# Performance work log

Hardware: AMD Instinct MI355X
Metric: run time of the kernel (lower is better)

## Reference

```python
import jax, jax.numpy as jnp
import numpy as np

B, N, E, S, ANN_D, N_STEPS = 16384, 70, 3, 10, 1, 5


def setup_inputs() -> dict:
    key = jax.random.key(0)
    ks = jax.random.split(key, 10)
    std = 0.02
    annotation = jax.random.normal(ks[0], (B, N), jnp.float32)
    A_raw = jax.random.uniform(ks[1], (N, N * E), jnp.float32) + 1e-3
    A = A_raw / A_raw.sum(axis=1, keepdims=True)  # row-normalized like torch.div(A, sum(A,1))
    W_in = jax.random.normal(ks[2], (E, S, S), jnp.float32) * std
    b_in = jnp.zeros((E, S), jnp.float32)
    Wr = jax.random.normal(ks[3], (S, 2 * S), jnp.float32) * std
    br = jnp.zeros((S,), jnp.float32)
    Wz = jax.random.normal(ks[4], (S, 2 * S), jnp.float32) * std
    bz = jnp.zeros((S,), jnp.float32)
    Wh = jax.random.normal(ks[5], (S, 2 * S), jnp.float32) * std
    bh = jnp.zeros((S,), jnp.float32)
    Wo1 = jax.random.normal(ks[6], (S, S + ANN_D), jnp.float32) * std
    bo1 = jnp.zeros((S,), jnp.float32)
    Wo2 = jax.random.normal(ks[7], (1, S), jnp.float32) * std
    bo2 = jnp.zeros((1,), jnp.float32)
    return {"annotation": annotation, "A": A, "W_in": W_in, "b_in": b_in,
            "Wr": Wr, "br": br, "Wz": Wz, "bz": bz, "Wh": Wh, "bh": bh,
            "Wo1": Wo1, "bo1": bo1, "Wo2": Wo2, "bo2": bo2}


def reference(annotation, A, W_in, b_in, Wr, br, Wz, bz, Wh, bh, Wo1, bo1, Wo2, bo2):
    b, n = annotation.shape
    ann = annotation[..., None]  # [B, N, 1]
    # initial state: annotation padded with zeros to state_dim
    prop = jnp.concatenate([ann, jnp.zeros((b, n, S - ANN_D), annotation.dtype)], axis=2)  # [B,N,S]
    for _ in range(N_STEPS):
        # per-edge-type linear: [B,E,N,S]; view order is edge-type-major (matches torch stack/transpose/view)
        ins = jnp.einsum('bnd,efd->benf', prop, W_in) + b_in[None, :, None, :]
        ins = ins.reshape(b, E * n, S)  # [B, E*N, S]
        a_in = jnp.einsum('nm,bms->bns', A, ins)  # bmm aggregation, [B,N,S]
        a = jnp.concatenate([a_in, prop], axis=2)  # [B,N,2S]
        r = jax.nn.sigmoid(a @ Wr.T + br)
        z = jax.nn.sigmoid(a @ Wz.T + bz)
        joined = jnp.concatenate([a_in, r * prop], axis=2)
        h_hat = jnp.tanh(joined @ Wh.T + bh)
        prop = (1.0 - z) * prop + z * h_hat
    join_state = jnp.concatenate([prop, ann], axis=2)  # [B,N,S+1]
    out = jnp.tanh(join_state @ Wo1.T + bo1) @ Wo2.T + bo2  # [B,N,1]
    return out.sum(axis=2)  # [B,N]
```

## Files before the change

### kernel.cpp

```cpp
#include <hip/hip_runtime.h>
#include <hip/hip_bf16.h>

typedef _Float16 v8h __attribute__((ext_vector_type(8)));
typedef _Float16 v4h __attribute__((ext_vector_type(4)));
typedef _Float16 v2h __attribute__((ext_vector_type(2)));
typedef float    v4f __attribute__((ext_vector_type(4)));

#define NTOT  16384
#define NN    70
#define STEPS 5
#define TPB   64
#define NBLK  NTOT
#define CATN  40
#define CATH  3208
#define USTR  232
#define UH    (10*USTR)

#define PWO1 0
#define PWO2 120
#define PBO2 130
#define NWP  132

#define OFR  1024
#define OFZ  1536
#define OFH  2048
#define OFA  2560
#define NWF  20480
#define PREPB 40

__device__ __align__(16) float    g_w[NWP];
__device__ __align__(16) _Float16 g_wf[NWF];
__device__ int g_flag;

__device__ __forceinline__ float fast_sigmoid(float x) {
    return __builtin_amdgcn_rcpf(1.0f + __expf(-x));
}
__device__ __forceinline__ float fast_tanh(float x) {
    float ax = fabsf(x);
    float e  = __expf(-2.0f * ax);
    float t  = (1.0f - e) * __builtin_amdgcn_rcpf(1.0f + e);
    return copysignf(t, x);
}

struct __align__(16) Smem {
    _Float16 U[UH];
    _Float16 cat[CATH];
};

__global__ void prep_kernel(const void* annv, const void* Av,
    const void* winv, const void* binv, const void* wrv, const void* brv,
    const void* wzv, const void* bzv, const void* whv, const void* bhv,
    const void* wo1v, const void* bo1v, const void* wo2v, const void* bo2v)
{
    __shared__ int sflag;
    if (threadIdx.x == 0) {
        const unsigned short* u = (const unsigned short*)annv;
        int good = 0;
        for (int k = 0; k < 128; ++k) {
            unsigned short bb = u[k];
            int ex = (bb >> 7) & 0xFF;
            if (bb == 0 || (ex >= 101 && ex <= 131)) ++good;
        }
        sflag = (good >= 112) ? 1 : 0;
        if (blockIdx.x == 0) g_flag = sflag;
    }
    __syncthreads();
    const int f = sflag;
    #define RD(p, i) (f ? (float)((const __hip_bfloat16*)(p))[i] : ((const float*)(p))[i])
    const int tid = threadIdx.x;
    if (blockIdx.x == 0) {
        for (int idx = tid; idx < 120; idx += blockDim.x) {
            const int s = idx / 12, cc = idx - s*12;
            g_w[PWO1 + idx] = (cc < 11) ? RD(wo1v, s*11 + cc) : RD(bo1v, s);
        }
        for (int idx = tid; idx < 10; idx += blockDim.x) g_w[PWO2 + idx] = RD(wo2v, idx);
        if (tid == 0) { g_w[PBO2] = RD(bo2v, 0); g_w[PBO2+1] = 0.f; }
    }
    for (int idx = blockIdx.x*blockDim.x + tid; idx < NWF; idx += gridDim.x*blockDim.x) {
        float val = 0.f;
        if (idx < OFR) {
            const int nt = idx >> 9, rem = idx & 511, lane = rem >> 3, j = rem & 7;
            const int k = ((lane >> 4) << 3) + j, col = nt*16 + (lane & 15);
            if (col < 30) {
                const int e = col / 10, s = col - e*10;
                if (k >= 16 && k < 26) val = RD(winv, e*100 + s*10 + (k-16));
                else if (k == 26)      val = RD(binv, e*10 + s);
            }
        } else if (idx < OFH) {
            const int i2 = idx - OFR;
            const int mt = i2 >> 9, rem = i2 & 511, lane = rem >> 3, j = rem & 7;
            const int k = ((lane >> 4) << 3) + j, s = lane & 15;
            if (s < 10) {
                const void* Wv = mt ? wzv : wrv;
                const void* bv = mt ? bzv : brv;
                if (k < 10)                 val = RD(Wv, s*20 + k);
                else if (k >= 16 && k < 26) val = RD(Wv, s*20 + 10 + (k-16));
                else if (k == 26)           val = RD(bv, s);
            }
        } else if (idx < OFA) {
            const int i2 = idx - OFH;
            const int lane = i2 >> 3, j = i2 & 7;
            const int k = ((lane >> 4) << 3) + j, s = lane & 15;
            if (s < 10) {
                if (k < 10)                 val = RD(whv, s*20 + k);
                else if (k >= 16 && k < 26) val = RD(whv, s*20 + 10 + (k-16));
                else if (k == 26)           val = RD(bhv, s);
            }
        } else {
            const int i2 = idx - OFA;
            const int w = i2 / 3584, rem = i2 - w*3584;
            const int kt = rem >> 9, r2 = rem & 511, lane = r2 >> 3, j = r2 & 7;
            const int m = w*16 + (lane & 15);
            const int k = kt*32 + ((lane >> 4) << 3) + j;
            const int e = k / 72, mm = k - e*72;
            if (m < NN && e < 3 && mm < NN) val = RD(Av, m*210 + e*70 + mm);
        }
        g_wf[idx] = (_Float16)val;
    }
    #undef RD
}

template<typename T>
__device__ __forceinline__ void run_impl(const void* annv, void* outv, Smem& sm)
{
    const T* ann_g = (const T*)annv;
    T* out_g       = (T*)outv;
    const int lane = threadIdx.x;
    const int blk  = blockIdx.x;
    const int q    = lane >> 4;
    const int c    = lane & 15;
    const float* __restrict__ gw = g_w;

    const v8h w1f0 = *(const v8h*)&g_wf[       lane*8];
    const v8h w1f1 = *(const v8h*)&g_wf[512  + lane*8];
    const v8h wrf  = *(const v8h*)&g_wf[OFR  + lane*8];
    const v8h wzf  = *(const v8h*)&g_wf[OFZ  + lane*8];
    const v8h whf  = *(const v8h*)&g_wf[OFH  + lane*8];
    v8h adj[35];
    #pragma unroll
    for (int i = 0; i < 35; ++i)
        adj[i] = *(const v8h*)&g_wf[OFA + i*512 + lane*8];

    {
        const int4 zz = {0,0,0,0};
        int4* z = (int4*)&sm;
        #pragma unroll 4
        for (int i = lane; i < (int)(sizeof(Smem)/16); i += TPB) z[i] = zz;
    }
    __syncthreads();

    for (int n2 = lane; n2 < NN; n2 += TPB) {
        sm.cat[n2*CATN + 16] = (_Float16)(float)ann_g[blk*NN + n2];
        sm.cat[n2*CATN + 26] = (_Float16)1.0f;
    }
    __syncthreads();

    #define PHASE1() do {                                                        \
        _Pragma("unroll")                                                        \
        for (int mt = 0; mt < 5; ++mt) {                                         \
            const v8h af = *(const v8h*)&sm.cat[(mt*16 + c)*CATN + q*8];         \
            const int node0 = mt*16 + q*4;                                       \
            _Pragma("unroll")                                                    \
            for (int nt = 0; nt < 2; ++nt) {                                     \
                v4f acc = {0.f,0.f,0.f,0.f};                                     \
                acc = __builtin_amdgcn_mfma_f32_16x16x32_f16(                    \
                        af, nt ? w1f1 : w1f0, acc, 0,0,0);                       \
                const int colw = nt*16 + c;                                      \
                if (colw < 30 && node0 <= 68) {                                  \
                    const int e = colw / 10, s = colw - e*10;                    \
                    v4h hv = {(_Float16)acc[0],(_Float16)acc[1],                 \
                              (_Float16)acc[2],(_Float16)acc[3]};                \
                    *(v4h*)&sm.U[s*USTR + e*72 + node0] = hv;                    \
                }                                                                \
            }                                                                    \
        }                                                                        \
    } while(0)

    PHASE1();
    __syncthreads();

    #pragma unroll 1
    for (int step = 0; step < STEPS; ++step) {
        {
            v8h bfr[7];
            #pragma unroll
            for (int kt = 0; kt < 7; ++kt)
                bfr[kt] = *(const v8h*)&sm.U[c*USTR + q*8 + kt*32];
            #pragma unroll
            for (int mt = 0; mt < 5; ++mt) {
                v4f acc = {0.f,0.f,0.f,0.f};
                #pragma unroll
                for (int kt = 0; kt < 7; ++kt)
                    acc = __builtin_amdgcn_mfma_f32_16x16x32_f16(
                        bfr[kt], adj[mt*7+kt], acc, 0,0,0);
                const int node = mt*16 + c;
                if (node < NN) {
                    const v4h hv = {(_Float16)acc[0],(_Float16)acc[1],
                                    (_Float16)acc[2],(_Float16)acc[3]};
                    _Float16* wp = &sm.cat[node*CATN + q*4];
                    if (q < 2)       *(v4h*)wp = hv;
                    else if (q == 2) *(v2h*)wp = (v2h){hv[0], hv[1]};
                }
            }
        }
        __syncthreads();

        v4h zgp[5], pgp[5];
        {
            #pragma unroll
            for (int nt = 0; nt < 5; ++nt) {
                const int node = nt*16 + c;
                const v8h bf = *(const v8h*)&sm.cat[node*CATN + q*8];
                v4f ar = {0.f,0.f,0.f,0.f}, az = {0.f,0.f,0.f,0.f};
                ar = __builtin_amdgcn_mfma_f32_16x16x32_f16(wrf, bf, ar, 0,0,0);
                az = __builtin_amdgcn_mfma_f32_16x16x32_f16(wzf, bf, az, 0,0,0);
                const v4h pv = *(const v4h*)&sm.cat[node*CATN + 16 + q*4];
                v4h rp, zh;
                #pragma unroll
                for (int i = 0; i < 4; ++i) {
                    const float p = (float)pv[i];
                    zh[i] = (_Float16)fast_sigmoid(az[i]);
                    rp[i] = (_Float16)(fast_sigmoid(ar[i]) * p);
                }
                zgp[nt] = zh; pgp[nt] = pv;
                if (node < NN) {
                    _Float16* wp = &sm.cat[node*CATN + 16 + q*4];
                    if (q < 2)       *(v4h*)wp = rp;
                    else if (q == 2) *(v2h*)wp = (v2h){rp[0], rp[1]};
                }
            }
        }
        __syncthreads();

        {
            #pragma unroll
            for (int nt = 0; nt < 5; ++nt) {
                const int node = nt*16 + c;
                const v8h bf2 = *(const v8h*)&sm.cat[node*CATN + q*8];
                v4f ah = {0.f,0.f,0.f,0.f};
                ah = __builtin_amdgcn_mfma_f32_16x16x32_f16(whf, bf2, ah, 0,0,0);
                v4h pn;
                #pragma unroll
                for (int i = 0; i < 4; ++i) {
                    const float hh = fast_tanh(ah[i]);
                    const float p  = (float)pgp[nt][i];
                    const float z  = (float)zgp[nt][i];
                    pn[i] = (_Float16)(p + z*(hh - p));
                }
                if (node < NN) {
                    _Float16* wp = &sm.cat[node*CATN + 16 + q*4];
                    if (q < 2)       *(v4h*)wp = pn;
                    else if (q == 2) *(v2h*)wp = (v2h){pn[0], pn[1]};
                }
            }
        }
        __syncthreads();

        if (step < STEPS-1) {
            PHASE1();
            __syncthreads();
        }
    }
    #undef PHASE1

    for (int n2 = lane; n2 < NN; n2 += TPB) {
        const _Float16* pc = &sm.cat[n2*CATN + 16];
        const v8h p8 = *(const v8h*)pc;
        const v2h p2 = *(const v2h*)(pc + 8);
        float pr[10];
        #pragma unroll
        for (int i = 0; i < 8; ++i) pr[i] = (float)p8[i];
        pr[8] = (float)p2[0]; pr[9] = (float)p2[1];
        const float av = (float)ann_g[blk*NN + n2];
        float o = gw[PBO2];
        #pragma unroll
        for (int s = 0; s < 10; ++s) {
            const float* wr_ = &gw[PWO1 + s*12];
            float acc = wr_[11] + wr_[10]*av;
            #pragma unroll
            for (int d = 0; d < 10; ++d) acc += pr[d]*wr_[d];
            o += fast_tanh(acc) * gw[PWO2 + s];
        }
        out_g[blk*NN + n2] = (T)o;
    }
}

__global__ __launch_bounds__(TPB, 2)
void ggnn_kernel(const void* annv, void* outv)
{
    __shared__ Smem sm;
    if (g_flag)
        run_impl<__hip_bfloat16>(annv, outv, sm);
    else
        run_impl<float>(annv, outv, sm);
}

extern "C" void kernel_launch(void* const* d_in, const int* in_sizes, int n_in,
                              void* d_out, int out_size, void* d_ws, size_t ws_size,
                              hipStream_t stream) {
    (void)in_sizes; (void)n_in; (void)out_size; (void)d_ws; (void)ws_size;
    hipLaunchKernelGGL(prep_kernel, dim3(PREPB), dim3(256), 0, stream,
        d_in[0], d_in[1], d_in[2], d_in[3], d_in[4], d_in[5], d_in[6],
        d_in[7], d_in[8], d_in[9], d_in[10], d_in[11], d_in[12], d_in[13]);
    hipLaunchKernelGGL(ggnn_kernel, dim3(NBLK), dim3(TPB), 0, stream,
        d_in[0], d_out);
}
```

Before: 267.8 us.

## Process two graphs per wavefront to amortize register-resident adjacency loads

Each 64-thread block now handles two batch graphs instead of one, using two shared-memory buffers and interleaving the MFMA streams for both graphs. The register-resident adjacency and weight fragments (35+ v8h loads per block) are reused across two graphs, which halves their global load cost and gives independent MFMA chains for latency hiding. In exchange, shared memory per block doubles and register pressure rises from the duplicated fragments, which could lower occupancy or cause spills under the launch bound of 2.

```diff
diff --git a/kernel.cpp b/kernel.cpp
--- a/kernel.cpp
+++ b/kernel.cpp
@@ -10,7 +10,8 @@
 #define NN    70
 #define STEPS 5
 #define TPB   64
-#define NBLK  NTOT
+#define GPW   2
+#define NBLK  (NTOT/GPW)
 #define CATN  40
 #define CATH  3208
 #define USTR  232
@@ -121,12 +122,12 @@
 }
 
 template<typename T>
-__device__ __forceinline__ void run_impl(const void* annv, void* outv, Smem& sm)
+__device__ __forceinline__ void run2(const void* annv, void* outv,
+                                     Smem& s0, Smem& s1, const int g0, const int g1)
 {
     const T* ann_g = (const T*)annv;
     T* out_g       = (T*)outv;
     const int lane = threadIdx.x;
-    const int blk  = blockIdx.x;
     const int q    = lane >> 4;
     const int c    = lane & 15;
     const float* __restrict__ gw = g_w;
@@ -143,34 +144,42 @@
 
     {
         const int4 zz = {0,0,0,0};
-        int4* z = (int4*)&sm;
+        int4* z0 = (int4*)&s0;
+        int4* z1 = (int4*)&s1;
         #pragma unroll 4
-        for (int i = lane; i < (int)(sizeof(Smem)/16); i += TPB) z[i] = zz;
+        for (int i = lane; i < (int)(sizeof(Smem)/16); i += TPB) { z0[i] = zz; z1[i] = zz; }
     }
     __syncthreads();
 
     for (int n2 = lane; n2 < NN; n2 += TPB) {
-        sm.cat[n2*CATN + 16] = (_Float16)(float)ann_g[blk*NN + n2];
-        sm.cat[n2*CATN + 26] = (_Float16)1.0f;
+        s0.cat[n2*CATN + 16] = (_Float16)(float)ann_g[g0*NN + n2];
+        s1.cat[n2*CATN + 16] = (_Float16)(float)ann_g[g1*NN + n2];
+        s0.cat[n2*CATN + 26] = (_Float16)1.0f;
+        s1.cat[n2*CATN + 26] = (_Float16)1.0f;
     }
     __syncthreads();
 
     #define PHASE1() do {                                                        \
         _Pragma("unroll")                                                        \
         for (int mt = 0; mt < 5; ++mt) {                                         \
-            const v8h af = *(const v8h*)&sm.cat[(mt*16 + c)*CATN + q*8];         \
+            const v8h af0 = *(const v8h*)&s0.cat[(mt*16 + c)*CATN + q*8];        \
+            const v8h af1 = *(const v8h*)&s1.cat[(mt*16 + c)*CATN + q*8];        \
             const int node0 = mt*16 + q*4;                                       \
             _Pragma("unroll")                                                    \
             for (int nt = 0; nt < 2; ++nt) {                                     \
-                v4f acc = {0.f,0.f,0.f,0.f};                                     \
-                acc = __builtin_amdgcn_mfma_f32_16x16x32_f16(                    \
-                        af, nt ? w1f1 : w1f0, acc, 0,0,0);                       \
+                const v8h wb = nt ? w1f1 : w1f0;                                 \
+                v4f a0 = {0.f,0.f,0.f,0.f}, a1 = {0.f,0.f,0.f,0.f};              \
+                a0 = __builtin_amdgcn_mfma_f32_16x16x32_f16(af0, wb, a0, 0,0,0); \
+                a1 = __builtin_amdgcn_mfma_f32_16x16x32_f16(af1, wb, a1, 0,0,0); \
                 const int colw = nt*16 + c;                                      \
                 if (colw < 30 && node0 <= 68) {                                  \
                     const int e = colw / 10, s = colw - e*10;                    \
-                    v4h hv = {(_Float16)acc[0],(_Float16)acc[1],                 \
-                              (_Float16)acc[2],(_Float16)acc[3]};                \
-                    *(v4h*)&sm.U[s*USTR + e*72 + node0] = hv;                    \
+                    *(v4h*)&s0.U[s*USTR + e*72 + node0] =                        \
+                        (v4h){(_Float16)a0[0],(_Float16)a0[1],                   \
+                              (_Float16)a0[2],(_Float16)a0[3]};                  \
+                    *(v4h*)&s1.U[s*USTR + e*72 + node0] =                        \
+                        (v4h){(_Float16)a1[0],(_Float16)a1[1],                   \
+                              (_Float16)a1[2],(_Float16)a1[3]};                  \
                 }                                                                \
             }                                                                    \
         }                                                                        \
@@ -182,51 +191,69 @@
     #pragma unroll 1
     for (int step = 0; step < STEPS; ++step) {
         {
-            v8h bfr[7];
-            #pragma unroll
-            for (int kt = 0; kt < 7; ++kt)
-                bfr[kt] = *(const v8h*)&sm.U[c*USTR + q*8 + kt*32];
+            v8h bfr0[7], bfr1[7];
+            #pragma unroll
+            for (int kt = 0; kt < 7; ++kt) {
+                bfr0[kt] = *(const v8h*)&s0.U[c*USTR + q*8 + kt*32];
+                bfr1[kt] = *(const v8h*)&s1.U[c*USTR + q*8 + kt*32];
+            }
             #pragma unroll
             for (int mt = 0; mt < 5; ++mt) {
-                v4f acc = {0.f,0.f,0.f,0.f};
+                v4f a0 = {0.f,0.f,0.f,0.f}, a1 = {0.f,0.f,0.f,0.f};
                 #pragma unroll
-                for (int kt = 0; kt < 7; ++kt)
-                    acc = __builtin_amdgcn_mfma_f32_16x16x32_f16(
-                        bfr[kt], adj[mt*7+kt], acc, 0,0,0);
+                for (int kt = 0; kt < 7; ++kt) {
+                    const v8h av = adj[mt*7+kt];
+                    a0 = __builtin_amdgcn_mfma_f32_16x16x32_f16(bfr0[kt], av, a0, 0,0,0);
+                    a1 = __builtin_amdgcn_mfma_f32_16x16x32_f16(bfr1[kt], av, a1, 0,0,0);
+                }
                 const int node = mt*16 + c;
                 if (node < NN) {
-                    const v4h hv = {(_Float16)acc[0],(_Float16)acc[1],
-                                    (_Float16)acc[2],(_Float16)acc[3]};
-                    _Float16* wp = &sm.cat[node*CATN + q*4];
-                    if (q < 2)       *(v4h*)wp = hv;
-                    else if (q == 2) *(v2h*)wp = (v2h){hv[0], hv[1]};
+                    const v4h h0 = {(_Float16)a0[0],(_Float16)a0[1],
+                                    (_Float16)a0[2],(_Float16)a0[3]};
+                    const v4h h1 = {(_Float16)a1[0],(_Float16)a1[1],
+                                    (_Float16)a1[2],(_Float16)a1[3]};
+                    _Float16* w0 = &s0.cat[node*CATN + q*4];
+                    _Float16* w1 = &s1.cat[node*CATN + q*4];
+                    if (q < 2)       { *(v4h*)w0 = h0; *(v4h*)w1 = h1; }
+                    else if (q == 2) { *(v2h*)w0 = (v2h){h0[0], h0[1]};
+                                       *(v2h*)w1 = (v2h){h1[0], h1[1]}; }
                 }
             }
         }
         __syncthreads();
 
-        v4h zgp[5], pgp[5];
+        v4h zgp0[5], pgp0[5], zgp1[5], pgp1[5];
         {
             #pragma unroll
             for (int nt = 0; nt < 5; ++nt) {
                 const int node = nt*16 + c;
-                const v8h bf = *(const v8h*)&sm.cat[node*CATN + q*8];
-                v4f ar = {0.f,0.f,0.f,0.f}, az = {0.f,0.f,0.f,0.f};
-                ar = __builtin_amdgcn_mfma_f32_16x16x32_f16(wrf, bf, ar, 0,0,0);
-                az = __builtin_amdgcn_mfma_f32_16x16x32_f16(wzf, bf, az, 0,0,0);
-                const v4h pv = *(const v4h*)&sm.cat[node*CATN + 16 + q*4];
-                v4h rp, zh;
+                const v8h bf0 = *(const v8h*)&s0.cat[node*CATN + q*8];
+                const v8h bf1 = *(const v8h*)&s1.cat[node*CATN + q*8];
+                v4f ar0 = {0.f,0.f,0.f,0.f}, az0 = {0.f,0.f,0.f,0.f};
+                v4f ar1 = {0.f,0.f,0.f,0.f}, az1 = {0.f,0.f,0.f,0.f};
+                ar0 = __builtin_amdgcn_mfma_f32_16x16x32_f16(wrf, bf0, ar0, 0,0,0);
+                ar1 = __builtin_amdgcn_mfma_f32_16x16x32_f16(wrf, bf1, ar1, 0,0,0);
+                az0 = __builtin_amdgcn_mfma_f32_16x16x32_f16(wzf, bf0, az0, 0,0,0);
+                az1 = __builtin_amdgcn_mfma_f32_16x16x32_f16(wzf, bf1, az1, 0,0,0);
+                const v4h pv0 = *(const v4h*)&s0.cat[node*CATN + 16 + q*4];
+                const v4h pv1 = *(const v4h*)&s1.cat[node*CATN + 16 + q*4];
+                v4h rp0, zh0, rp1, zh1;
                 #pragma unroll
                 for (int i = 0; i < 4; ++i) {
-                    const float p = (float)pv[i];
-                    zh[i] = (_Float16)fast_sigmoid(az[i]);
-                    rp[i] = (_Float16)(fast_sigmoid(ar[i]) * p);
-                }
-                zgp[nt] = zh; pgp[nt] = pv;
+                    const float p0 = (float)pv0[i], p1 = (float)pv1[i];
+                    zh0[i] = (_Float16)fast_sigmoid(az0[i]);
+                    zh1[i] = (_Float16)fast_sigmoid(az1[i]);
+                    rp0[i] = (_Float16)(fast_sigmoid(ar0[i]) * p0);
+                    rp1[i] = (_Float16)(fast_sigmoid(ar1[i]) * p1);
+                }
+                zgp0[nt] = zh0; pgp0[nt] = pv0;
+                zgp1[nt] = zh1; pgp1[nt] = pv1;
                 if (node < NN) {
-                    _Float16* wp = &sm.cat[node*CATN + 16 + q*4];
-                    if (q < 2)       *(v4h*)wp = rp;
-                    else if (q == 2) *(v2h*)wp = (v2h){rp[0], rp[1]};
+                    _Float16* w0 = &s0.cat[node*CATN + 16 + q*4];
+                    _Float16* w1 = &s1.cat[node*CATN + 16 + q*4];
+                    if (q < 2)       { *(v4h*)w0 = rp0; *(v4h*)w1 = rp1; }
+                    else if (q == 2) { *(v2h*)w0 = (v2h){rp0[0], rp0[1]};
+                                       *(v2h*)w1 = (v2h){rp1[0], rp1[1]}; }
                 }
             }
         }
@@ -236,21 +263,27 @@
             #pragma unroll
             for (int nt = 0; nt < 5; ++nt) {
                 const int node = nt*16 + c;
-                const v8h bf2 = *(const v8h*)&sm.cat[node*CATN + q*8];
-                v4f ah = {0.f,0.f,0.f,0.f};
-                ah = __builtin_amdgcn_mfma_f32_16x16x32_f16(whf, bf2, ah, 0,0,0);
-                v4h pn;
+                const v8h bf0 = *(const v8h*)&s0.cat[node*CATN + q*8];
+                const v8h bf1 = *(const v8h*)&s1.cat[node*CATN + q*8];
+                v4f ah0 = {0.f,0.f,0.f,0.f}, ah1 = {0.f,0.f,0.f,0.f};
+                ah0 = __builtin_amdgcn_mfma_f32_16x16x32_f16(whf, bf0, ah0, 0,0,0);
+                ah1 = __builtin_amdgcn_mfma_f32_16x16x32_f16(whf, bf1, ah1, 0,0,0);
+                v4h pn0, pn1;
                 #pragma unroll
                 for (int i = 0; i < 4; ++i) {
-                    const float hh = fast_tanh(ah[i]);
-                    const float p  = (float)pgp[nt][i];
-                    const float z  = (float)zgp[nt][i];
-                    pn[i] = (_Float16)(p + z*(hh - p));
+                    const float h0 = fast_tanh(ah0[i]);
+                    const float h1 = fast_tanh(ah1[i]);
+                    const float p0 = (float)pgp0[nt][i], z0 = (float)zgp0[nt][i];
+                    const float p1 = (float)pgp1[nt][i], z1 = (float)zgp1[nt][i];
+                    pn0[i] = (_Float16)(p0 + z0*(h0 - p0));
+                    pn1[i] = (_Float16)(p1 + z1*(h1 - p1));
                 }
                 if (node < NN) {
-                    _Float16* wp = &sm.cat[node*CATN + 16 + q*4];
-                    if (q < 2)       *(v4h*)wp = pn;
-                    else if (q == 2) *(v2h*)wp = (v2h){pn[0], pn[1]};
+                    _Float16* w0 = &s0.cat[node*CATN + 16 + q*4];
+                    _Float16* w1 = &s1.cat[node*CATN + 16 + q*4];
+                    if (q < 2)       { *(v4h*)w0 = pn0; *(v4h*)w1 = pn1; }
+                    else if (q == 2) { *(v2h*)w0 = (v2h){pn0[0], pn0[1]};
+                                       *(v2h*)w1 = (v2h){pn1[0], pn1[1]}; }
                 }
             }
         }
@@ -264,35 +297,48 @@
     #undef PHASE1
 
     for (int n2 = lane; n2 < NN; n2 += TPB) {
-        const _Float16* pc = &sm.cat[n2*CATN + 16];
-        const v8h p8 = *(const v8h*)pc;
-        const v2h p2 = *(const v2h*)(pc + 8);
-        float pr[10];
-        #pragma unroll
-        for (int i = 0; i < 8; ++i) pr[i] = (float)p8[i];
-        pr[8] = (float)p2[0]; pr[9] = (float)p2[1];
-        const float av = (float)ann_g[blk*NN + n2];
-        float o = gw[PBO2];
+        const float av0 = (float)ann_g[g0*NN + n2];
+        const float av1 = (float)ann_g[g1*NN + n2];
+        float pr0[10], pr1[10];
+        {
+            const v8h p8 = *(const v8h*)&s0.cat[n2*CATN + 16];
+            const v2h p2 = *(const v2h*)&s0.cat[n2*CATN + 24];
+            #pragma unroll
+            for (int i = 0; i < 8; ++i) pr0[i] = (float)p8[i];
+            pr0[8] = (float)p2[0]; pr0[9] = (float)p2[1];
+        }
+        {
+            const v8h p8 = *(const v8h*)&s1.cat[n2*CATN + 16];
+            const v2h p2 = *(const v2h*)&s1.cat[n2*CATN + 24];
+            #pragma unroll
+            for (int i = 0; i < 8; ++i) pr1[i] = (float)p8[i];
+            pr1[8] = (float)p2[0]; pr1[9] = (float)p2[1];
+        }
+        float o0 = gw[PBO2], o1 = gw[PBO2];
         #pragma unroll
         for (int s = 0; s < 10; ++s) {
             const float* wr_ = &gw[PWO1 + s*12];
-            float acc = wr_[11] + wr_[10]*av;
-            #pragma unroll
-            for (int d = 0; d < 10; ++d) acc += pr[d]*wr_[d];
-            o += fast_tanh(acc) * gw[PWO2 + s];
-        }
-        out_g[blk*NN + n2] = (T)o;
+            float a0 = wr_[11] + wr_[10]*av0;
+            float a1 = wr_[11] + wr_[10]*av1;
+            #pragma unroll
+            for (int d = 0; d < 10; ++d) { a0 += pr0[d]*wr_[d]; a1 += pr1[d]*wr_[d]; }
+            o0 += fast_tanh(a0) * gw[PWO2 + s];
+            o1 += fast_tanh(a1) * gw[PWO2 + s];
+        }
+        out_g[g0*NN + n2] = (T)o0;
+        out_g[g1*NN + n2] = (T)o1;
     }
 }
 
 __global__ __launch_bounds__(TPB, 2)
 void ggnn_kernel(const void* annv, void* outv)
 {
-    __shared__ Smem sm;
+    __shared__ Smem sm0, sm1;
+    const int g0 = blockIdx.x * GPW;
     if (g_flag)
-        run_impl<__hip_bfloat16>(annv, outv, sm);
+        run2<__hip_bfloat16>(annv, outv, sm0, sm1, g0, g0+1);
     else
-        run_impl<float>(annv, outv, sm);
+        run2<float>(annv, outv, sm0, sm1, g0, g0+1);
 }
 
 extern "C" void kernel_launch(void* const* d_in, const int* in_sizes, int n_in,
```

Result: slower. 285.5 us (+6.6%).

## Fuse GRU gate and candidate phases via lane permutes, drop a barrier

Applied to the files above, without the earlier changes.

Builds the r*prop operand for the candidate MFMA directly in registers. It uses ds_bpermute cross-lane shuffles instead of writing r*prop to shared memory and re-reading it after a barrier, which removes one __syncthreads and one LDS round trip per step. Gate values stay in fp32 registers instead of being rounded to fp16. Float-to-half conversions now use packed round-toward-zero instructions, which slightly changes rounding behaviour. The lane-permute layout is intricate and carries a correctness risk if the fragment mapping is wrong.

```diff
diff --git a/kernel.cpp b/kernel.cpp
--- a/kernel.cpp
+++ b/kernel.cpp
@@ -5,6 +5,8 @@
 typedef _Float16 v4h __attribute__((ext_vector_type(4)));
 typedef _Float16 v2h __attribute__((ext_vector_type(2)));
 typedef float    v4f __attribute__((ext_vector_type(4)));
+typedef int      v4i __attribute__((ext_vector_type(4)));
+typedef int      v2i __attribute__((ext_vector_type(2)));
 
 #define NTOT  16384
 #define NN    70
@@ -40,6 +42,12 @@
     float e  = __expf(-2.0f * ax);
     float t  = (1.0f - e) * __builtin_amdgcn_rcpf(1.0f + e);
     return copysignf(t, x);
+}
+__device__ __forceinline__ v4h pk4(v4f a) {
+    auto lo = __builtin_amdgcn_cvt_pkrtz(a[0], a[1]);
+    auto hi = __builtin_amdgcn_cvt_pkrtz(a[2], a[3]);
+    v4h r; r[0] = lo[0]; r[1] = lo[1]; r[2] = hi[0]; r[3] = hi[1];
+    return r;
 }
 
 struct __align__(16) Smem {
@@ -141,6 +149,10 @@
     for (int i = 0; i < 35; ++i)
         adj[i] = *(const v8h*)&g_wf[OFA + i*512 + lane*8];
 
+    const int a_lo  = c << 2;
+    const int a_mid = (16 + c) << 2;
+    const int a_sel = (q == 3) ? ((32 + c) << 2) : a_lo;
+
     {
         const int4 zz = {0,0,0,0};
         int4* z = (int4*)&sm;
@@ -168,9 +180,7 @@
                 const int colw = nt*16 + c;                                      \
                 if (colw < 30 && node0 <= 68) {                                  \
                     const int e = colw / 10, s = colw - e*10;                    \
-                    v4h hv = {(_Float16)acc[0],(_Float16)acc[1],                 \
-                              (_Float16)acc[2],(_Float16)acc[3]};                \
-                    *(v4h*)&sm.U[s*USTR + e*72 + node0] = hv;                    \
+                    *(v4h*)&sm.U[s*USTR + e*72 + node0] = pk4(acc);              \
                 }                                                                \
             }                                                                    \
         }                                                                        \
@@ -195,8 +205,7 @@
                         bfr[kt], adj[mt*7+kt], acc, 0,0,0);
                 const int node = mt*16 + c;
                 if (node < NN) {
-                    const v4h hv = {(_Float16)acc[0],(_Float16)acc[1],
-                                    (_Float16)acc[2],(_Float16)acc[3]};
+                    const v4h hv = pk4(acc);
                     _Float16* wp = &sm.cat[node*CATN + q*4];
                     if (q < 2)       *(v4h*)wp = hv;
                     else if (q == 2) *(v2h*)wp = (v2h){hv[0], hv[1]};
@@ -205,7 +214,6 @@
         }
         __syncthreads();
 
-        v4h zgp[5], pgp[5];
         {
             #pragma unroll
             for (int nt = 0; nt < 5; ++nt) {
@@ -215,37 +223,34 @@
                 ar = __builtin_amdgcn_mfma_f32_16x16x32_f16(wrf, bf, ar, 0,0,0);
                 az = __builtin_amdgcn_mfma_f32_16x16x32_f16(wzf, bf, az, 0,0,0);
                 const v4h pv = *(const v4h*)&sm.cat[node*CATN + 16 + q*4];
-                v4h rp, zh;
+                float pg[4], zg[4];
+                v4f rpf;
                 #pragma unroll
                 for (int i = 0; i < 4; ++i) {
-                    const float p = (float)pv[i];
-                    zh[i] = (_Float16)fast_sigmoid(az[i]);
-                    rp[i] = (_Float16)(fast_sigmoid(ar[i]) * p);
+                    pg[i]  = (float)pv[i];
+                    zg[i]  = fast_sigmoid(az[i]);
+                    rpf[i] = fast_sigmoid(ar[i]) * pg[i];
                 }
-                zgp[nt] = zh; pgp[nt] = pv;
-                if (node < NN) {
-                    _Float16* wp = &sm.cat[node*CATN + 16 + q*4];
-                    if (q < 2)       *(v4h*)wp = rp;
-                    else if (q == 2) *(v2h*)wp = (v2h){rp[0], rp[1]};
-                }
-            }
-        }
-        __syncthreads();
-
-        {
-            #pragma unroll
-            for (int nt = 0; nt < 5; ++nt) {
-                const int node = nt*16 + c;
-                const v8h bf2 = *(const v8h*)&sm.cat[node*CATN + q*8];
+                const v4h rp = pk4(rpf);
+                const v2i rpi = __builtin_bit_cast(v2i, rp);
+                const int d0 = __builtin_amdgcn_ds_bpermute(a_sel, rpi[0]);
+                const int d1 = __builtin_amdgcn_ds_bpermute(a_lo,  rpi[1]);
+                const int d2 = __builtin_amdgcn_ds_bpermute(a_mid, rpi[0]);
+                const int d3 = __builtin_amdgcn_ds_bpermute(a_mid, rpi[1]);
+                const v4i bfi = __builtin_bit_cast(v4i, bf);
+                v4i b2;
+                b2[0] = (q < 2) ? bfi[0] : d0;
+                b2[1] = (q < 2) ? bfi[1] : ((q == 2) ? d1 : 0x00003C00);
+                b2[2] = (q < 2) ? bfi[2] : ((q == 2) ? d2 : 0);
+                b2[3] = (q < 2) ? bfi[3] : ((q == 2) ? d3 : 0);
+                const v8h bf2 = __builtin_bit_cast(v8h, b2);
                 v4f ah = {0.f,0.f,0.f,0.f};
                 ah = __builtin_amdgcn_mfma_f32_16x16x32_f16(whf, bf2, ah, 0,0,0);
                 v4h pn;
                 #pragma unroll
                 for (int i = 0; i < 4; ++i) {
                     const float hh = fast_tanh(ah[i]);
-                    const float p  = (float)pgp[nt][i];
-                    const float z  = (float)zgp[nt][i];
-                    pn[i] = (_Float16)(p + z*(hh - p));
+                    pn[i] = (_Float16)(pg[i] + zg[i]*(hh - pg[i]));
                 }
                 if (node < NN) {
                     _Float16* wp = &sm.cat[node*CATN + 16 + q*4];
```

Result: faster. 259.2 us (-3.2%).
